# Kernel tuning notes

Measured on AMD Instinct MI355X. Metric: run time of the kernel, lower is better.

## Reference

```python
import jax, jax.numpy as jnp
import numpy as np

N = 65536  # number of points
# (out_ch, in_ch) for the 8 shared-MLP (1x1-conv) blocks
_DIMS = [(64, 3), (64, 64), (128, 64), (1024, 128), (512, 1088), (256, 512), (128, 256), (1, 128)]


def setup_inputs() -> dict:
    key = jax.random.key(0)
    ks = jax.random.split(key, 1 + 2 * len(_DIMS))
    inp = {"x": jax.random.normal(ks[0], (1, 1, N, 3), jnp.float32)}
    for i, (o, c) in enumerate(_DIMS):
        scale = 1.0 / np.sqrt(c)
        inp[f"W{i+1}"] = jax.random.normal(ks[1 + 2 * i], (o, c), jnp.float32) * scale
        inp[f"b{i+1}"] = jax.random.uniform(ks[2 + 2 * i], (o,), jnp.float32, -scale, scale)
    return inp


def reference(x, W1, b1, W2, b2, W3, b3, W4, b4, W5, b5, W6, b6, W7, b7, W8, b8):
    # x: [1,1,n,3]. Conv2d with kernel [1,3] over the width-3 axis == per-point linear on xyz.
    pts = x[0, 0]                                   # [n,3]
    n = pts.shape[0]
    h = jax.nn.relu(pts @ W1.T + b1)                # [n,64]   block1
    h = jax.nn.relu(h @ W2.T + b2)                  # [n,64]   block2 (kept for skip-concat)
    y = jax.nn.relu(h @ W3.T + b3)                  # [n,128]  block3
    y = jax.nn.relu(y @ W4.T + b4)                  # [n,1024] block4
    g = jnp.max(y, axis=0)                          # [1024]   global max-pool over points
    # broadcast global feature to every point and concat with per-point features -> [n,1088]
    feat = jnp.concatenate([h, jnp.broadcast_to(g, (n, g.shape[0]))], axis=1)
    z = jax.nn.relu(feat @ W5.T + b5)               # [n,512]
    z = jax.nn.relu(z @ W6.T + b6)                  # [n,256]
    z = jax.nn.relu(z @ W7.T + b7)                  # [n,128]
    z = z @ W8.T + b8                               # [n,1]    block8 (no relu)
    return z.reshape(1, 1, n, 1)
```

## Files before the change

kernel.cpp:

```cpp
#include <hip/hip_runtime.h>

#define NPTS 65536

typedef __bf16 bf16_t;
typedef __bf16 bf16x8 __attribute__((ext_vector_type(8)));
typedef float f32x16 __attribute__((ext_vector_type(16)));

#define MFMA32(A, B, C) __builtin_amdgcn_mfma_f32_32x32x16_bf16(A, B, C, 0, 0, 0)

__device__ __forceinline__ float relu(float v) { return v > 0.f ? v : 0.f; }


struct PrepSeg { const float* src; bf16_t* h; bf16_t* l; int SW; int K; int nblk; };
struct PrepAll { PrepSeg seg[6]; };

__global__ __launch_bounds__(256, 2) void kprep_k1a(
    PrepAll pa,
    const float* __restrict__ x, const float* __restrict__ W1, const float* __restrict__ b1,
    bf16_t* __restrict__ h1h, bf16_t* __restrict__ h1l) {
  if (blockIdx.x < 166) {
    int blk = blockIdx.x, i = 0;
    while (blk >= pa.seg[i].nblk) { blk -= pa.seg[i].nblk; ++i; }
    const PrepSeg sg = pa.seg[i];
    int t8 = blk * 256 + threadIdx.x;
    int l = t8 & 63;
    int rest = t8 >> 6;
    int NKC = sg.K >> 4;
    int kc = rest % NKC, st = rest / NKC;
    int n = st * 32 + (l & 31);
    int k0 = kc * 16 + (l >> 5) * 8;
    const float* src = sg.src + (size_t)n * sg.SW + k0;
    bf16x8 hv, lv;
#pragma unroll
    for (int j = 0; j < 8; ++j) {
      float v = src[j];
      bf16_t h = (bf16_t)v;
      hv[j] = h; lv[j] = (bf16_t)(v - (float)h);
    }
    *(bf16x8*)(sg.h + (size_t)t8 * 8) = hv;
    *(bf16x8*)(sg.l + (size_t)t8 * 8) = lv;
  } else {
    int p = (blockIdx.x - 166) * 256 + threadIdx.x;
    float x0 = x[p * 3 + 0], x1 = x[p * 3 + 1], x2 = x[p * 3 + 2];
    int b = p >> 7, mi = (p >> 5) & 3, p31 = p & 31;
#pragma unroll
    for (int kc = 0; kc < 4; ++kc)
#pragma unroll
      for (int hbw = 0; hbw < 2; ++hbw) {
        bf16x8 hv, lv;
#pragma unroll
        for (int j = 0; j < 8; ++j) {
          int c = kc * 16 + hbw * 8 + j;
          float v = relu(fmaf(W1[c * 3], x0, fmaf(W1[c * 3 + 1], x1, fmaf(W1[c * 3 + 2], x2, b1[c]))));
          bf16_t h = (bf16_t)v;
          hv[j] = h; lv[j] = (bf16_t)(v - (float)h);
        }
        size_t off = (((size_t)(b * 4 + kc) * 4 + mi) * 64 + hbw * 32 + p31) * 8;
        *(bf16x8*)(h1h + off) = hv;
        *(bf16x8*)(h1l + off) = lv;
      }
  }
}

struct Oct { bf16x8 h0, l0, h1, l1; };
__device__ __forceinline__ Oct epi_pack(const f32x16& accv, int hb) {
  float a[16], rcv[8];
#pragma unroll
  for (int r = 0; r < 16; ++r) a[r] = relu(accv[r]);
#pragma unroll
  for (int j = 0; j < 8; ++j) rcv[j] = __shfl_xor(hb ? a[j] : a[8 + j], 32);
  float o0[8], o1[8];
#pragma unroll
  for (int j = 0; j < 4; ++j) {
    o0[j]     = hb ? rcv[j]     : a[j];
    o0[4 + j] = hb ? a[8 + j]   : rcv[j];
    o1[j]     = hb ? rcv[4 + j] : a[4 + j];
    o1[4 + j] = hb ? a[12 + j]  : rcv[4 + j];
  }
  Oct o;
#pragma unroll
  for (int j = 0; j < 8; ++j) {
    bf16_t x0 = (bf16_t)o0[j]; o.h0[j] = x0; o.l0[j] = (bf16_t)(o0[j] - (float)x0);
    bf16_t x1 = (bf16_t)o1[j]; o.h1[j] = x1; o.l1[j] = (bf16_t)(o1[j] - (float)x1);
  }
  return o;
}

__device__ __forceinline__ void epi_store_lds(const Oct& o, bf16_t* H, bf16_t* L, int ob, int p31) {
  *(bf16x8*)(H + (ob + p31) * 8)      = o.h0;
  *(bf16x8*)(H + (ob + 32 + p31) * 8) = o.h1;
  *(bf16x8*)(L + (ob + p31) * 8)      = o.l0;
  *(bf16x8*)(L + (ob + 32 + p31) * 8) = o.l1;
}

__device__ __forceinline__ void binit2(f32x16 acc[2], const float* bias, int base, int hb) {
#pragma unroll
  for (int r = 0; r < 16; ++r) {
    float bv = bias[base + 8 * (r >> 2) + 4 * hb + (r & 3)];
    acc[0][r] = bv; acc[1][r] = bv;
  }
}

template <int PB, int K, int MODE>
__global__ __launch_bounds__(256, 3) void gemmS(
    const bf16_t* __restrict__ Ah, const bf16_t* __restrict__ Al,
    const bf16_t* __restrict__ Wh, const bf16_t* __restrict__ Wl,
    const float* __restrict__ bias, int nko,
    bf16_t* __restrict__ Oh, bf16_t* __restrict__ Ol,
    float* __restrict__ aux, const float* __restrict__ w8, const float* __restrict__ b8) {
  constexpr int WC = 4 / PB;
  constexpr int NKC = K / 16;
  constexpr int KG = 2;
  constexpr int NG = NKC / KG;
  __shared__ bf16_t smem[2][PB][2][KG * 2048];

  int tid = threadIdx.x;
  int lane = tid & 63;
  int w = __builtin_amdgcn_readfirstlane(tid >> 6);
  int rg = w / WC, cw = w % WC;
  int hb = lane >> 5, p31 = lane & 31;
  int bx = blockIdx.x;
  int st0 = blockIdx.y * WC + cw;
  int bblk = bx * PB + rg;

  f32x16 acc[4];
#pragma unroll
  for (int r = 0; r < 16; ++r) {
    float bv = bias[st0 * 32 + 8 * (r >> 2) + 4 * hb + (r & 3)];
#pragma unroll
    for (int mi = 0; mi < 4; ++mi) acc[mi][r] = bv;
  }

  auto stage = [&](int buf, int g) {
#pragma unroll
    for (int i = 0; i < PB * 4; ++i) {
      int u = i * 256 + tid;
      int rgs = u >> 10, rem = u & 1023;
      int t = rem >> 9, inner = rem & 511;
      const bf16_t* src = (t ? Al : Ah) +
          ((size_t)(bx * PB + rgs) * NKC + g * KG) * 2048 + inner * 8;
      *(bf16x8*)&smem[buf][rgs][t][inner * 8] = *(const bf16x8*)src;
    }
  };

  bf16x8 wch[KG], wcl[KG], wnh[KG], wnl[KG];
  auto wload = [&](int g, bf16x8* h, bf16x8* l) {
#pragma unroll
    for (int kcl = 0; kcl < KG; ++kcl) {
      size_t wo = (((size_t)st0 * NKC + g * KG + kcl) * 64 + lane) * 8;
      h[kcl] = *(const bf16x8*)(Wh + wo);
      l[kcl] = *(const bf16x8*)(Wl + wo);
    }
  };

  auto compute = [&](int buf, bf16x8* h, bf16x8* l) {
#pragma unroll
    for (int kcl = 0; kcl < KG; ++kcl)
#pragma unroll
      for (int mi = 0; mi < 4; ++mi) {
        const bf16_t* xp = &smem[buf][rg][0][((kcl * 4 + mi) * 64 + lane) * 8];
        bf16x8 xh = *(const bf16x8*)xp;
        bf16x8 xl = *(const bf16x8*)(xp + KG * 2048);
        acc[mi] = MFMA32(h[kcl], xh, acc[mi]);
        acc[mi] = MFMA32(l[kcl], xh, acc[mi]);
        acc[mi] = MFMA32(h[kcl], xl, acc[mi]);
      }
  };

  stage(0, 0);
  wload(0, wch, wcl);
  for (int g = 0; g < NG; ++g) {
    __syncthreads();
    if (g + 1 < NG) {
      stage((g + 1) & 1, g + 1);
      wload(g + 1, wnh, wnl);
    }
    compute(g & 1, wch, wcl);
#pragma unroll
    for (int kcl = 0; kcl < KG; ++kcl) { wch[kcl] = wnh[kcl]; wcl[kcl] = wnl[kcl]; }
  }

  if constexpr (MODE == 0) {
#pragma unroll
    for (int mi = 0; mi < 4; ++mi) {
      Oct o = epi_pack(acc[mi], hb);
      int kco = st0 * 2 + hb;
      size_t ob = ((size_t)(bblk * nko + kco) * 4 + mi) * 64;
      *(bf16x8*)(Oh + (ob + p31) * 8)      = o.h0;
      *(bf16x8*)(Ol + (ob + p31) * 8)      = o.l0;
      *(bf16x8*)(Oh + (ob + 32 + p31) * 8) = o.h1;
      *(bf16x8*)(Ol + (ob + 32 + p31) * 8) = o.l1;
    }
  } else if constexpr (MODE == 1) {
#pragma unroll
    for (int r = 0; r < 16; ++r) {
      float m = relu(acc[0][r]);
#pragma unroll
      for (int mi = 1; mi < 4; ++mi) m = fmaxf(m, relu(acc[mi][r]));
#pragma unroll
      for (int off = 1; off < 32; off <<= 1) m = fmaxf(m, __shfl_xor(m, off));
      if (p31 == 0)
        aux[(size_t)bx * 1024 + st0 * 32 + 8 * (r >> 2) + 4 * hb + (r & 3)] = m;
    }
  } else {
    __shared__ float sp[4][128];
    float w8v[16];
#pragma unroll
    for (int r = 0; r < 16; ++r) w8v[r] = w8[st0 * 32 + 8 * (r >> 2) + 4 * hb + (r & 3)];
#pragma unroll
    for (int mi = 0; mi < 4; ++mi) {
      float s = 0.f;
#pragma unroll
      for (int r = 0; r < 16; ++r) s = fmaf(relu(acc[mi][r]), w8v[r], s);
      s += __shfl_xor(s, 32);
      if (hb == 0) sp[w][mi * 32 + p31] = s;
    }
    __syncthreads();
    if (tid < 128)
      aux[(size_t)bx * 128 + tid] = sp[0][tid] + sp[1][tid] + sp[2][tid] + sp[3][tid] + b8[0];
  }
}

__global__ __launch_bounds__(512, 1) void kl34max(
    const bf16_t* __restrict__ h2h, const bf16_t* __restrict__ h2l,
    const bf16_t* __restrict__ W3h, const bf16_t* __restrict__ W3l,
    const float* __restrict__ b3,
    const bf16_t* __restrict__ Wh, const bf16_t* __restrict__ Wl,
    const float* __restrict__ bias, float* __restrict__ gpart) {
  __shared__ __align__(16) bf16_t sA[81920];
  bf16_t* wq = sA + 65536;
  int tid = threadIdx.x, lane = tid & 63;
  int w = __builtin_amdgcn_readfirstlane(tid >> 6);
  int w3 = w & 3, t = w >> 2;
  int hb = lane >> 5, p31 = lane & 31;
  int bx = blockIdx.x;
  int pb = bx * 2 + t;
  int rot = (bx >> 2) & 7;
  bf16_t* sT = sA + t * 32768;

  auto issueW = [&](int u) {
    int jj = u >> 2, kp = (u & 3) * 2;
#pragma unroll
    for (int i = 0; i < 2; ++i) {
      int unit = i * 8 + w;
      int sslot = unit & 3;
      int q     = (unit >> 2) & 1;
      int part  = unit >> 3;
      int st = ((jj + rot) & 7) * 4 + sslot;
      int kc = kp + q;
      const bf16_t* W = part ? Wl : Wh;
      const bf16_t* gp = W + ((size_t)(st * 8 + kc) * 64 + lane) * 8;
      bf16_t* lp = wq + (u & 1) * 8192 + (sslot * 4 + q * 2 + part) * 512;
      __builtin_amdgcn_global_load_lds(
          (const __attribute__((address_space(1))) void*)gp,
          (__attribute__((address_space(3))) void*)lp, 16, 0, 0);
    }
  };
  issueW(0);

  {
    bf16x8 hx[4], lx[4];
#pragma unroll
    for (int kc = 0; kc < 4; ++kc) {
      size_t so = (((size_t)(pb * 4 + kc) * 4 + w3) * 64 + lane) * 8;
      hx[kc] = *(const bf16x8*)(h2h + so);
      lx[kc] = *(const bf16x8*)(h2l + so);
    }
#pragma unroll
    for (int spr = 0; spr < 2; ++spr) {
      f32x16 a3[2];
#pragma unroll
      for (int s = 0; s < 2; ++s) {
        int st = spr * 2 + s;
#pragma unroll
        for (int r = 0; r < 16; ++r)
          a3[s][r] = b3[st * 32 + 8 * (r >> 2) + 4 * hb + (r & 3)];
      }
#pragma unroll
      for (int kc = 0; kc < 4; ++kc)
#pragma unroll
        for (int s = 0; s < 2; ++s) {
          int st = spr * 2 + s;
          size_t wo = ((size_t)(st * 4 + kc) * 64 + lane) * 8;
          bf16x8 wh3 = *(const bf16x8*)(W3h + wo);
          bf16x8 wl3 = *(const bf16x8*)(W3l + wo);
          a3[s] = MFMA32(wh3, hx[kc], a3[s]);
          a3[s] = MFMA32(wl3, hx[kc], a3[s]);
          a3[s] = MFMA32(wh3, lx[kc], a3[s]);
        }
#pragma unroll
      for (int s = 0; s < 2; ++s) {
        int st = spr * 2 + s;
        Oct o = epi_pack(a3[s], hb);
        epi_store_lds(o, sT, sT + 16384, ((st * 2 + hb) * 4 + w3) * 64, p31);
      }
    }
  }
  __syncthreads();

  f32x16 acc[4];
#pragma unroll 1
  for (int u = 0; u < 32; ++u) {
    asm volatile("s_waitcnt vmcnt(0)" ::: "memory");
    __builtin_amdgcn_sched_barrier(0);
    __builtin_amdgcn_s_barrier();
    if (u + 1 < 32) issueW(u + 1);
    int jj = u >> 2, kp = (u & 3) * 2;
    int stc = ((jj + rot) & 7) * 4 + w3;
    if ((u & 3) == 0) {
#pragma unroll
      for (int r = 0; r < 16; ++r) {
        float bv = bias[stc * 32 + 8 * (r >> 2) + 4 * hb + (r & 3)];
#pragma unroll
        for (int mi = 0; mi < 4; ++mi) acc[mi][r] = bv;
      }
    }
    const bf16_t* wb = wq + (u & 1) * 8192;
#pragma unroll
    for (int q = 0; q < 2; ++q) {
      int kc = kp + q;
      bf16x8 cwh = *(const bf16x8*)(wb + (w3 * 4 + q * 2) * 512 + lane * 8);
      bf16x8 cwl = *(const bf16x8*)(wb + (w3 * 4 + q * 2 + 1) * 512 + lane * 8);
      __builtin_amdgcn_s_setprio(1);
#pragma unroll
      for (int mi = 0; mi < 4; ++mi) {
        const bf16_t* xp = sT + ((kc * 4 + mi) * 64 + lane) * 8;
        bf16x8 xh = *(const bf16x8*)xp;
        bf16x8 xl = *(const bf16x8*)(xp + 16384);
        acc[mi] = MFMA32(cwh, xh, acc[mi]);
        acc[mi] = MFMA32(cwl, xh, acc[mi]);
        acc[mi] = MFMA32(cwh, xl, acc[mi]);
      }
      __builtin_amdgcn_s_setprio(0);
    }
    if ((u & 3) == 3) {
#pragma unroll
      for (int r = 0; r < 16; ++r) {
        float m = fmaxf(fmaxf(acc[0][r], acc[1][r]), fmaxf(acc[2][r], acc[3][r]));
        m = fmaxf(m, 0.f);
#pragma unroll
        for (int off = 1; off < 32; off <<= 1) m = fmaxf(m, __shfl_xor(m, off));
        if (p31 == 0)
          gpart[(size_t)pb * 1024 + stc * 32 + 8 * (r >> 2) + 4 * hb + (r & 3)] = m;
      }
    }
  }
}

__global__ __launch_bounds__(256) void kgmax(const float* __restrict__ gpart, float* __restrict__ g) {
  int t = blockIdx.x * 256 + threadIdx.x;
  int c = t & 1023, rg = t >> 10;
  const float* gp = gpart + (size_t)rg * 64 * 1024 + c;
  float m = 0.f;
#pragma unroll 8
  for (int r = 0; r < 64; ++r) m = fmaxf(m, gp[(size_t)r * 1024]);
  atomicMax((unsigned int*)(g + c), __float_as_uint(m));
}

__global__ __launch_bounds__(256) void kc5(
    const float* __restrict__ W5, const float* __restrict__ b5,
    const float* __restrict__ g, float* __restrict__ c5) {
  int lane = threadIdx.x & 63;
  int wv = blockIdx.x * 4 + (threadIdx.x >> 6);
  float gv[16];
#pragma unroll
  for (int k = 0; k < 16; ++k) gv[k] = g[k * 64 + lane];
#pragma unroll
  for (int i = 0; i < 4; ++i) {
    int c = wv * 4 + i;
    const float* wrow = W5 + (size_t)c * 1088 + 64;
    float acc = 0.f;
#pragma unroll
    for (int k = 0; k < 16; ++k) acc = fmaf(wrow[k * 64 + lane], gv[k], acc);
#pragma unroll
    for (int off = 1; off < 64; off <<= 1) acc += __shfl_xor(acc, off);
    if (lane == 0) c5[c] = acc + b5[c];
  }
}


__global__ __launch_bounds__(256, 2) void mega2(
    const bf16_t* __restrict__ h2gh, const bf16_t* __restrict__ h2gl,
    const bf16_t* __restrict__ W5h, const bf16_t* __restrict__ W5l, const float* __restrict__ c5,
    const bf16_t* __restrict__ W6h, const bf16_t* __restrict__ W6l, const float* __restrict__ b6,
    const bf16_t* __restrict__ W7h, const bf16_t* __restrict__ W7l, const float* __restrict__ b7,
    const float* __restrict__ w8, const float* __restrict__ b8v, float* __restrict__ out) {
  __shared__ __align__(16) bf16_t smem[32768];
  __shared__ float sp[4][64];
  int tid = threadIdx.x, lane = tid & 63;
  int w = __builtin_amdgcn_readfirstlane(tid >> 6);
  int hb = lane >> 5, p31 = lane & 31;
  int b = blockIdx.x;
  int B = b >> 1, half = b & 1;

  bf16x8 xh[4][2], xl[4][2];
#pragma unroll
  for (int kc = 0; kc < 4; ++kc)
#pragma unroll
    for (int mi = 0; mi < 2; ++mi) {
      size_t so = (((size_t)((B * 4 + kc) * 4 + half * 2 + mi)) * 64 + lane) * 8;
      xh[kc][mi] = *(const bf16x8*)(h2gh + so);
      xl[kc][mi] = *(const bf16x8*)(h2gl + so);
    }

  f32x16 z6a[2][2];
#pragma unroll
  for (int s = 0; s < 2; ++s)
#pragma unroll
    for (int r = 0; r < 16; ++r) {
      float bv = b6[(w * 2 + s) * 32 + 8 * (r >> 2) + 4 * hb + (r & 3)];
      z6a[s][0][r] = bv; z6a[s][1][r] = bv;
    }

  bf16x8 w5h[4], w5l[4];
  auto w5load = [&](int g) {
#pragma unroll
    for (int kc = 0; kc < 4; ++kc) {
      size_t wo = (((size_t)(g * 4 + w) * 4 + kc) * 64 + lane) * 8;
      w5h[kc] = *(const bf16x8*)(W5h + wo);
      w5l[kc] = *(const bf16x8*)(W5l + wo);
    }
  };
  w5load(0);

  bf16x8 w6p[3][2][2];
  auto w6loadp = [&](int g, int kc, int slot) {
#pragma unroll
    for (int s = 0; s < 2; ++s) {
      size_t wo = ((size_t)((w * 2 + s) * 32 + g * 8 + kc) * 64 + lane) * 8;
      w6p[slot][s][0] = *(const bf16x8*)(W6h + wo);
      w6p[slot][s][1] = *(const bf16x8*)(W6l + wo);
    }
  };

  for (int g5 = 0; g5 < 4; ++g5) {
    bf16_t* zbuf = smem + (g5 & 1) * 16384;
    int st5 = g5 * 4 + w;
    f32x16 a5[2];
    binit2(a5, c5, st5 * 32, hb);
    __builtin_amdgcn_s_setprio(1);
#pragma unroll
    for (int kc = 0; kc < 4; ++kc) {
#pragma unroll
      for (int mi = 0; mi < 2; ++mi) a5[mi] = MFMA32(w5h[kc], xh[kc][mi], a5[mi]);
#pragma unroll
      for (int mi = 0; mi < 2; ++mi) a5[mi] = MFMA32(w5l[kc], xh[kc][mi], a5[mi]);
#pragma unroll
      for (int mi = 0; mi < 2; ++mi) a5[mi] = MFMA32(w5h[kc], xl[kc][mi], a5[mi]);
    }
    __builtin_amdgcn_s_setprio(0);
    if (g5 < 3) w5load(g5 + 1);
#pragma unroll
    for (int mi = 0; mi < 2; ++mi) {
      Oct o = epi_pack(a5[mi], hb);
      epi_store_lds(o, zbuf, zbuf + 8192, ((w * 2 + hb) * 2 + mi) * 64, p31);
    }
    w6loadp(g5, 0, 0);
    w6loadp(g5, 1, 1);
    __syncthreads();
#pragma unroll
    for (int kc = 0; kc < 8; ++kc) {
      if (kc + 2 < 8) w6loadp(g5, kc + 2, (kc + 2) % 3);
      bf16x8 zxh[2], zxl[2];
#pragma unroll
      for (int mi = 0; mi < 2; ++mi) {
        const bf16_t* xp = zbuf + ((kc * 2 + mi) * 64 + lane) * 8;
        zxh[mi] = *(const bf16x8*)xp;
        zxl[mi] = *(const bf16x8*)(xp + 8192);
      }
      __builtin_amdgcn_s_setprio(1);
#pragma unroll
      for (int s = 0; s < 2; ++s)
#pragma unroll
        for (int mi = 0; mi < 2; ++mi) z6a[s][mi] = MFMA32(w6p[kc % 3][s][0], zxh[mi], z6a[s][mi]);
#pragma unroll
      for (int s = 0; s < 2; ++s)
#pragma unroll
        for (int mi = 0; mi < 2; ++mi) z6a[s][mi] = MFMA32(w6p[kc % 3][s][1], zxh[mi], z6a[s][mi]);
#pragma unroll
      for (int s = 0; s < 2; ++s)
#pragma unroll
        for (int mi = 0; mi < 2; ++mi) z6a[s][mi] = MFMA32(w6p[kc % 3][s][0], zxl[mi], z6a[s][mi]);
      __builtin_amdgcn_s_setprio(0);
    }
  }
  __syncthreads();
#pragma unroll
  for (int s = 0; s < 2; ++s) {
    int kcb = (w * 2 + s) * 2 + hb;
#pragma unroll
    for (int mi = 0; mi < 2; ++mi) {
      Oct o = epi_pack(z6a[s][mi], hb);
      epi_store_lds(o, smem, smem + 16384, (kcb * 2 + mi) * 64, p31);
    }
  }
  bf16x8 w7p[3][2];
  auto w7loadp = [&](int kc, int slot) {
    size_t wo = ((size_t)(w * 16 + kc) * 64 + lane) * 8;
    w7p[slot][0] = *(const bf16x8*)(W7h + wo);
    w7p[slot][1] = *(const bf16x8*)(W7l + wo);
  };
  w7loadp(0, 0);
  w7loadp(1, 1);
  __syncthreads();
  f32x16 a7[2];
  binit2(a7, b7, w * 32, hb);
#pragma unroll
  for (int kc = 0; kc < 16; ++kc) {
    if (kc + 2 < 16) w7loadp(kc + 2, (kc + 2) % 3);
    bf16x8 zxh[2], zxl[2];
#pragma unroll
    for (int mi = 0; mi < 2; ++mi) {
      const bf16_t* xp = smem + ((kc * 2 + mi) * 64 + lane) * 8;
      zxh[mi] = *(const bf16x8*)xp;
      zxl[mi] = *(const bf16x8*)(xp + 16384);
    }
    __builtin_amdgcn_s_setprio(1);
#pragma unroll
    for (int mi = 0; mi < 2; ++mi) a7[mi] = MFMA32(w7p[kc % 3][0], zxh[mi], a7[mi]);
#pragma unroll
    for (int mi = 0; mi < 2; ++mi) a7[mi] = MFMA32(w7p[kc % 3][1], zxh[mi], a7[mi]);
#pragma unroll
    for (int mi = 0; mi < 2; ++mi) a7[mi] = MFMA32(w7p[kc % 3][0], zxl[mi], a7[mi]);
    __builtin_amdgcn_s_setprio(0);
  }
  float w8v[16];
#pragma unroll
  for (int r = 0; r < 16; ++r) w8v[r] = w8[w * 32 + 8 * (r >> 2) + 4 * hb + (r & 3)];
#pragma unroll
  for (int mi = 0; mi < 2; ++mi) {
    float s = 0.f;
#pragma unroll
    for (int r = 0; r < 16; ++r) s = fmaf(relu(a7[mi][r]), w8v[r], s);
    s += __shfl_xor(s, 32);
    if (hb == 0) sp[w][mi * 32 + p31] = s;
  }
  __syncthreads();
  if (tid < 64)
    out[b * 64 + tid] = sp[0][tid] + sp[1][tid] + sp[2][tid] + sp[3][tid] + b8v[0];
}

extern "C" void kernel_launch(void* const* d_in, const int* in_sizes, int n_in,
                              void* d_out, int out_size, void* d_ws, size_t ws_size,
                              hipStream_t stream) {
  const float* x  = (const float*)d_in[0];
  const float* W1 = (const float*)d_in[1];  const float* b1 = (const float*)d_in[2];
  const float* W2 = (const float*)d_in[3];  const float* b2 = (const float*)d_in[4];
  const float* W3 = (const float*)d_in[5];  const float* b3 = (const float*)d_in[6];
  const float* W4 = (const float*)d_in[7];  const float* b4 = (const float*)d_in[8];
  const float* W5 = (const float*)d_in[9];  const float* b5 = (const float*)d_in[10];
  const float* W6 = (const float*)d_in[11]; const float* b6 = (const float*)d_in[12];
  const float* W7 = (const float*)d_in[13]; const float* b7 = (const float*)d_in[14];
  const float* W8 = (const float*)d_in[15]; const float* b8 = (const float*)d_in[16];
  float* out = (float*)d_out;

  const size_t MB = 1ull << 20;
  char* ws = (char*)d_ws;
  bf16_t* h2h = (bf16_t*)(ws + 128 * MB);  bf16_t* h2l = (bf16_t*)(ws + 136 * MB);
  bf16_t* h1h = (bf16_t*)(ws + 144 * MB);  bf16_t* h1l = (bf16_t*)(ws + 152 * MB);
  float* gpart = (float*)(ws + 208 * MB);
  float* g     = (float*)(ws + 210 * MB);
  float* c5    = (float*)(ws + 210 * MB + 4096);
  char* wb = ws + 210 * MB + 65536;
  bf16_t* W2h = (bf16_t*)(wb);             bf16_t* W2l = (bf16_t*)(wb + 8192);
  bf16_t* W3h = (bf16_t*)(wb + 16384);     bf16_t* W3l = (bf16_t*)(wb + 32768);
  bf16_t* W4h = (bf16_t*)(wb + 49152);     bf16_t* W4l = (bf16_t*)(wb + 311296);
  bf16_t* W5h = (bf16_t*)(wb + 573440);    bf16_t* W5l = (bf16_t*)(wb + 638976);
  bf16_t* W6h = (bf16_t*)(wb + 704512);    bf16_t* W6l = (bf16_t*)(wb + 966656);
  bf16_t* W7h = (bf16_t*)(wb + 1228800);   bf16_t* W7l = (bf16_t*)(wb + 1294336);

  hipMemsetAsync(g, 0, 1024 * sizeof(float), stream);

  PrepAll pa;
  pa.seg[0] = {W2, W2h, W2l, 64, 64, 2};
  pa.seg[1] = {W3, W3h, W3l, 64, 64, 4};
  pa.seg[2] = {W4, W4h, W4l, 128, 128, 64};
  pa.seg[3] = {W5, W5h, W5l, 1088, 64, 16};
  pa.seg[4] = {W6, W6h, W6l, 512, 512, 64};
  pa.seg[5] = {W7, W7h, W7l, 256, 256, 16};

  kprep_k1a<<<422, 256, 0, stream>>>(pa, x, W1, b1, h1h, h1l);
  gemmS<2, 64, 0><<<dim3(256, 1), 256, 0, stream>>>(
      h1h, h1l, W2h, W2l, b2, 4, h2h, h2l, nullptr, nullptr, nullptr);
  kl34max<<<256, 512, 0, stream>>>(h2h, h2l, W3h, W3l, b3, W4h, W4l, b4, gpart);
  kgmax<<<32, 256, 0, stream>>>(gpart, g);
  kc5<<<32, 256, 0, stream>>>(W5, b5, g, c5);
  mega2<<<1024, 256, 0, stream>>>(h2h, h2l, W5h, W5l, c5, W6h, W6l, b6,
                                  W7h, W7l, b7, W8, b8, out);
}
```

Baseline: 248.2 us.

## Split fused layer3/4 max kernel into 256-thread blocks, one point tile each

The fused layer3/layer4/max-pool kernel previously ran 512-thread blocks in which two groups of four waves shared each staged weight chunk across two 128-point tiles. It now runs 256-thread blocks (twice as many), each owning a single point tile, with half the LDS and launch bounds allowing two blocks per CU. This aims for more resident blocks and better latency hiding. The cost is that each block streams the W4 weights on its own, doubling global weight traffic, and the loop runs 64 barrier-synchronized steps with one k-chunk each instead of 32 steps with two.

New measurement: 272.2 us. 9.7% more time.

```diff
diff --git a/kernel.cpp b/kernel.cpp
--- a/kernel.cpp
+++ b/kernel.cpp
@@ -221,36 +221,28 @@
   }
 }
 
-__global__ __launch_bounds__(512, 1) void kl34max(
+__global__ __launch_bounds__(256, 2) void kl34max(
     const bf16_t* __restrict__ h2h, const bf16_t* __restrict__ h2l,
     const bf16_t* __restrict__ W3h, const bf16_t* __restrict__ W3l,
     const float* __restrict__ b3,
     const bf16_t* __restrict__ Wh, const bf16_t* __restrict__ Wl,
     const float* __restrict__ bias, float* __restrict__ gpart) {
-  __shared__ __align__(16) bf16_t sA[81920];
-  bf16_t* wq = sA + 65536;
+  __shared__ __align__(16) bf16_t sA[40960];
+  bf16_t* wq = sA + 32768;
   int tid = threadIdx.x, lane = tid & 63;
   int w = __builtin_amdgcn_readfirstlane(tid >> 6);
-  int w3 = w & 3, t = w >> 2;
   int hb = lane >> 5, p31 = lane & 31;
   int bx = blockIdx.x;
-  int pb = bx * 2 + t;
   int rot = (bx >> 2) & 7;
-  bf16_t* sT = sA + t * 32768;
 
   auto issueW = [&](int u) {
-    int jj = u >> 2, kp = (u & 3) * 2;
+    int jj = u >> 3, kc = u & 7;
+    int st = ((jj + rot) & 7) * 4 + w;
 #pragma unroll
     for (int i = 0; i < 2; ++i) {
-      int unit = i * 8 + w;
-      int sslot = unit & 3;
-      int q     = (unit >> 2) & 1;
-      int part  = unit >> 3;
-      int st = ((jj + rot) & 7) * 4 + sslot;
-      int kc = kp + q;
-      const bf16_t* W = part ? Wl : Wh;
+      const bf16_t* W = i ? Wl : Wh;
       const bf16_t* gp = W + ((size_t)(st * 8 + kc) * 64 + lane) * 8;
-      bf16_t* lp = wq + (u & 1) * 8192 + (sslot * 4 + q * 2 + part) * 512;
+      bf16_t* lp = wq + (u & 1) * 4096 + (w * 2 + i) * 512;
       __builtin_amdgcn_global_load_lds(
           (const __attribute__((address_space(1))) void*)gp,
           (__attribute__((address_space(3))) void*)lp, 16, 0, 0);
@@ -262,7 +254,7 @@
     bf16x8 hx[4], lx[4];
 #pragma unroll
     for (int kc = 0; kc < 4; ++kc) {
-      size_t so = (((size_t)(pb * 4 + kc) * 4 + w3) * 64 + lane) * 8;
+      size_t so = (((size_t)(bx * 4 + kc) * 4 + w) * 64 + lane) * 8;
       hx[kc] = *(const bf16x8*)(h2h + so);
       lx[kc] = *(const bf16x8*)(h2l + so);
     }
@@ -292,7 +284,7 @@
       for (int s = 0; s < 2; ++s) {
         int st = spr * 2 + s;
         Oct o = epi_pack(a3[s], hb);
-        epi_store_lds(o, sT, sT + 16384, ((st * 2 + hb) * 4 + w3) * 64, p31);
+        epi_store_lds(o, sA, sA + 16384, ((st * 2 + hb) * 4 + w) * 64, p31);
       }
     }
   }
@@ -300,14 +292,14 @@
 
   f32x16 acc[4];
 #pragma unroll 1
-  for (int u = 0; u < 32; ++u) {
+  for (int u = 0; u < 64; ++u) {
     asm volatile("s_waitcnt vmcnt(0)" ::: "memory");
     __builtin_amdgcn_sched_barrier(0);
     __builtin_amdgcn_s_barrier();
-    if (u + 1 < 32) issueW(u + 1);
-    int jj = u >> 2, kp = (u & 3) * 2;
-    int stc = ((jj + rot) & 7) * 4 + w3;
-    if ((u & 3) == 0) {
+    if (u + 1 < 64) issueW(u + 1);
+    int jj = u >> 3, kc = u & 7;
+    int stc = ((jj + rot) & 7) * 4 + w;
+    if (kc == 0) {
 #pragma unroll
       for (int r = 0; r < 16; ++r) {
         float bv = bias[stc * 32 + 8 * (r >> 2) + 4 * hb + (r & 3)];
@@ -315,25 +307,21 @@
         for (int mi = 0; mi < 4; ++mi) acc[mi][r] = bv;
       }
     }
-    const bf16_t* wb = wq + (u & 1) * 8192;
-#pragma unroll
-    for (int q = 0; q < 2; ++q) {
-      int kc = kp + q;
-      bf16x8 cwh = *(const bf16x8*)(wb + (w3 * 4 + q * 2) * 512 + lane * 8);
-      bf16x8 cwl = *(const bf16x8*)(wb + (w3 * 4 + q * 2 + 1) * 512 + lane * 8);
-      __builtin_amdgcn_s_setprio(1);
-#pragma unroll
-      for (int mi = 0; mi < 4; ++mi) {
-        const bf16_t* xp = sT + ((kc * 4 + mi) * 64 + lane) * 8;
-        bf16x8 xh = *(const bf16x8*)xp;
-        bf16x8 xl = *(const bf16x8*)(xp + 16384);
-        acc[mi] = MFMA32(cwh, xh, acc[mi]);
-        acc[mi] = MFMA32(cwl, xh, acc[mi]);
-        acc[mi] = MFMA32(cwh, xl, acc[mi]);
-      }
-      __builtin_amdgcn_s_setprio(0);
-    }
-    if ((u & 3) == 3) {
+    const bf16_t* wb = wq + (u & 1) * 4096;
+    bf16x8 cwh = *(const bf16x8*)(wb + (w * 2 + 0) * 512 + lane * 8);
+    bf16x8 cwl = *(const bf16x8*)(wb + (w * 2 + 1) * 512 + lane * 8);
+    __builtin_amdgcn_s_setprio(1);
+#pragma unroll
+    for (int mi = 0; mi < 4; ++mi) {
+      const bf16_t* xp = sA + ((kc * 4 + mi) * 64 + lane) * 8;
+      bf16x8 xh = *(const bf16x8*)xp;
+      bf16x8 xl = *(const bf16x8*)(xp + 16384);
+      acc[mi] = MFMA32(cwh, xh, acc[mi]);
+      acc[mi] = MFMA32(cwl, xh, acc[mi]);
+      acc[mi] = MFMA32(cwh, xl, acc[mi]);
+    }
+    __builtin_amdgcn_s_setprio(0);
+    if (kc == 7) {
 #pragma unroll
       for (int r = 0; r < 16; ++r) {
         float m = fmaxf(fmaxf(acc[0][r], acc[1][r]), fmaxf(acc[2][r], acc[3][r]));
@@ -341,7 +329,7 @@
 #pragma unroll
         for (int off = 1; off < 32; off <<= 1) m = fmaxf(m, __shfl_xor(m, off));
         if (p31 == 0)
-          gpart[(size_t)pb * 1024 + stc * 32 + 8 * (r >> 2) + 4 * hb + (r & 3)] = m;
+          gpart[(size_t)bx * 1024 + stc * 32 + 8 * (r >> 2) + 4 * hb + (r & 3)] = m;
       }
     }
   }
@@ -582,7 +570,7 @@
   kprep_k1a<<<422, 256, 0, stream>>>(pa, x, W1, b1, h1h, h1l);
   gemmS<2, 64, 0><<<dim3(256, 1), 256, 0, stream>>>(
       h1h, h1l, W2h, W2l, b2, 4, h2h, h2l, nullptr, nullptr, nullptr);
-  kl34max<<<256, 512, 0, stream>>>(h2h, h2l, W3h, W3l, b3, W4h, W4l, b4, gpart);
+  kl34max<<<512, 256, 0, stream>>>(h2h, h2l, W3h, W3l, b3, W4h, W4l, b4, gpart);
   kgmax<<<32, 256, 0, stream>>>(gpart, g);
   kc5<<<32, 256, 0, stream>>>(W5, b5, g, c5);
   mega2<<<1024, 256, 0, stream>>>(h2h, h2l, W5h, W5l, c5, W6h, W6l, b6,
```
